# Kernel optimization log

Measured on AMD Instinct MI355X. Metric: run time of the kernel, lower is better.

## Reference

```python
import math
import jax, jax.numpy as jnp
import numpy as np

D_MODEL = 1024
N_HEADS = 16
D_HEAD = D_MODEL // N_HEADS


def get_alibi_slopes(n_heads: int) -> np.ndarray:
    def pow2_slopes(n):
        start = 2 ** (-2 ** (-(math.log2(n) - 3)))
        return np.array([start * start ** i for i in range(n)], dtype=np.float32)
    if math.log2(n_heads).is_integer():
        return pow2_slopes(n_heads)
    closest = 2 ** math.floor(math.log2(n_heads))
    slopes = pow2_slopes(closest)
    extra = pow2_slopes(2 * closest)[0::2][: n_heads - closest]
    return np.concatenate([slopes, extra], axis=0)


def setup_inputs() -> dict:
    key = jax.random.key(0)
    ks = jax.random.split(key, 9)
    B, S, D = 2, 2048, D_MODEL
    scale = 1.0 / math.sqrt(D)
    inp = {
        "x": jax.random.normal(ks[0], (B, S, D), dtype=jnp.float32),
        "Wq": jax.random.normal(ks[1], (D, D), dtype=jnp.float32) * scale,
        "bq": jnp.zeros((D,), dtype=jnp.float32),
        "Wk": jax.random.normal(ks[2], (D, D), dtype=jnp.float32) * scale,
        "bk": jnp.zeros((D,), dtype=jnp.float32),
        "Wv": jax.random.normal(ks[3], (D, D), dtype=jnp.float32) * scale,
        "bv": jnp.zeros((D,), dtype=jnp.float32),
        "Wo": jax.random.normal(ks[4], (D, D), dtype=jnp.float32) * scale,
        "bo": jnp.zeros((D,), dtype=jnp.float32),
    }
    return inp


def reference(x, Wq, bq, Wk, bk, Wv, bv, Wo, bo):
    B, S, D = x.shape
    H, Dh = N_HEADS, D_HEAD
    # projections (torch Linear: x @ W.T + b)
    q = (x @ Wq.T + bq).reshape(B, S, H, Dh).transpose(0, 2, 1, 3)  # [B,H,S,Dh]
    k = (x @ Wk.T + bk).reshape(B, S, H, Dh).transpose(0, 2, 1, 3)
    v = (x @ Wv.T + bv).reshape(B, S, H, Dh).transpose(0, 2, 1, 3)

    scores = jnp.einsum("bhqd,bhkd->bhqk", q, k) / math.sqrt(Dh)  # [B,H,S,S]

    slopes = jnp.asarray(get_alibi_slopes(H), dtype=scores.dtype)  # [H]
    pos = jnp.arange(S, dtype=scores.dtype)
    pos_diff = pos[None, :] - pos[:, None]                         # [S,S] (k - q)
    alibi = slopes[:, None, None] * pos_diff[None, :, :]           # [H,S,S]
    scores = scores + alibi[None]

    causal = jnp.tril(jnp.ones((S, S), dtype=bool))
    scores = jnp.where(causal[None, None], scores, -jnp.inf)

    weights = jax.nn.softmax(scores, axis=-1)
    y = jnp.einsum("bhqk,bhkd->bhqd", weights, v)                  # [B,H,S,Dh]
    y = y.transpose(0, 2, 1, 3).reshape(B, S, D)
    return y @ Wo.T + bo
```

## Files before the change

### kernel.cpp

```cpp
#include <hip/hip_runtime.h>

typedef unsigned short u16;
typedef unsigned int u32;
typedef short bf16x8 __attribute__((ext_vector_type(8)));
typedef float f32x4 __attribute__((ext_vector_type(4)));
typedef u16 u16x4 __attribute__((ext_vector_type(4)));

#define D_MODEL 1024
#define NHEADS 16
#define DHEAD 64
#define BATCH 2
#define SEQ 2048
#define NROWS (BATCH * SEQ)
#define NTILES (SEQ / 64)

static __device__ __forceinline__ u16 f2bf(float f) {
  u32 x = __float_as_uint(f);
  x += 0x7fffu + ((x >> 16) & 1u);
  return (u16)(x >> 16);
}

#define GLL16(gp, lp)                                             \
  __builtin_amdgcn_global_load_lds(                               \
      (const __attribute__((address_space(1))) u32*)(gp),         \
      (__attribute__((address_space(3))) u32*)(lp), 16, 0, 0)

__global__ __launch_bounds__(256) void castk(const float* __restrict__ in,
                                             u16* __restrict__ out, int n4) {
  int i = blockIdx.x * 256 + threadIdx.x;
  if (i >= n4) return;
  float4 v = ((const float4*)in)[i];
  u32 lo = (u32)f2bf(v.x) | ((u32)f2bf(v.y) << 16);
  u32 hi = (u32)f2bf(v.z) | ((u32)f2bf(v.w) << 16);
  ((uint2*)out)[i] = make_uint2(lo, hi);
}

__global__ __launch_bounds__(256) void castw(const float* __restrict__ w0,
                                             const float* __restrict__ w1,
                                             const float* __restrict__ w2,
                                             const float* __restrict__ w3,
                                             u16* __restrict__ o0,
                                             u16* __restrict__ o1,
                                             u16* __restrict__ o2,
                                             u16* __restrict__ o3) {
  const int z = blockIdx.z;
  const float* in = (z == 0) ? w0 : (z == 1) ? w1 : (z == 2) ? w2 : w3;
  u16* out = (z == 0) ? o0 : (z == 1) ? o1 : (z == 2) ? o2 : o3;
  int i = blockIdx.x * 256 + threadIdx.x;
  float4 v = ((const float4*)in)[i];
  u32 lo = (u32)f2bf(v.x) | ((u32)f2bf(v.y) << 16);
  u32 hi = (u32)f2bf(v.z) | ((u32)f2bf(v.w) << 16);
  ((uint2*)out)[i] = make_uint2(lo, hi);
}

template <int MODE>
__device__ __forceinline__ void gemm_core(const u16* __restrict__ A,
                                          const u16* __restrict__ Bw,
                                          const float* __restrict__ bias,
                                          u16* __restrict__ ob,
                                          float* __restrict__ of,
                                          int bm, int bn) {
  constexpr int K = 1024, N = 1024;
  __shared__ __attribute__((aligned(16))) u16 As[2][128 * 32];
  __shared__ __attribute__((aligned(16))) u16 Bs[2][128 * 32];
  const int tx = threadIdx.x;
  const int w = tx >> 6, lane = tx & 63;
  const int wm = w >> 1, wn = w & 1;
  const int c = lane & 15, g = lane >> 4;
  f32x4 acc[4][4];
  for (int m = 0; m < 4; ++m)
    for (int n = 0; n < 4; ++n) acc[m][n] = {0.f, 0.f, 0.f, 0.f};
  const int srow = w * 16 + (lane >> 2);
  const int sck = (lane & 3) * 8;
  for (int m = 0; m < 2; ++m) {
    GLL16(A + (size_t)(bm + m * 64 + srow) * K + sck,
          (char*)As[0] + m * 4096 + w * 1024);
    GLL16(Bw + (size_t)(bn + m * 64 + srow) * K + sck,
          (char*)Bs[0] + m * 4096 + w * 1024);
  }
  int cur = 0;
  for (int k0 = 0; k0 < K; k0 += 32) {
    __syncthreads();
    if (k0 + 32 < K) {
      for (int m = 0; m < 2; ++m) {
        GLL16(A + (size_t)(bm + m * 64 + srow) * K + k0 + 32 + sck,
              (char*)As[cur ^ 1] + m * 4096 + w * 1024);
        GLL16(Bw + (size_t)(bn + m * 64 + srow) * K + k0 + 32 + sck,
              (char*)Bs[cur ^ 1] + m * 4096 + w * 1024);
      }
    }
    bf16x8 af[4], bf_[4];
    for (int m = 0; m < 4; ++m)
      af[m] = *(const bf16x8*)(As[cur] + (wm * 64 + m * 16 + c) * 32 + g * 8);
    for (int n = 0; n < 4; ++n)
      bf_[n] = *(const bf16x8*)(Bs[cur] + (wn * 64 + n * 16 + c) * 32 + g * 8);
    for (int m = 0; m < 4; ++m)
      for (int n = 0; n < 4; ++n)
        acc[m][n] = __builtin_amdgcn_mfma_f32_16x16x32_bf16(af[m], bf_[n],
                                                            acc[m][n], 0, 0, 0);
    cur ^= 1;
  }
  for (int n = 0; n < 4; ++n) {
    const int col = bn + wn * 64 + n * 16 + c;
    const float bv = bias[col];
    for (int m = 0; m < 4; ++m) {
      if (MODE == 2) {
        const int rs = bm + wm * 64 + m * 16 + g * 4;
        u16x4 pk;
        for (int r = 0; r < 4; ++r) pk[r] = f2bf(acc[m][n][r] + bv);
        const size_t vrow = (size_t)((rs >> 11) * NHEADS + (col >> 6)) * DHEAD +
                            (col & 63);
        *(u16x4*)(ob + vrow * SEQ + (rs & 2047)) = pk;
      } else {
        for (int r = 0; r < 4; ++r) {
          const int row = bm + wm * 64 + m * 16 + g * 4 + r;
          float v = acc[m][n][r] + bv;
          if (MODE == 1)
            of[(size_t)row * N + col] = v;
          else
            ob[(size_t)row * N + col] = f2bf(v);
        }
      }
    }
  }
}

__global__ __launch_bounds__(256) void gemm_qkv(const u16* __restrict__ xb,
                                                const u16* __restrict__ wq,
                                                const u16* __restrict__ wk,
                                                const float* __restrict__ bq,
                                                const float* __restrict__ bk,
                                                u16* __restrict__ q,
                                                u16* __restrict__ k) {
  const int z = blockIdx.z;
  const u16* W = (z == 0) ? wq : wk;
  const float* bi = (z == 0) ? bq : bk;
  u16* o = (z == 0) ? q : k;
  gemm_core<0>(xb, W, bi, o, nullptr, blockIdx.y * 128, blockIdx.x * 128);
}

__global__ __launch_bounds__(256) void gemm_v(const u16* __restrict__ xb,
                                              const u16* __restrict__ wv,
                                              const float* __restrict__ bv,
                                              u16* __restrict__ vt) {
  gemm_core<2>(xb, wv, bv, vt, nullptr, blockIdx.y * 128, blockIdx.x * 128);
}

__global__ __launch_bounds__(256) void gemm_o(const u16* __restrict__ yb,
                                              const u16* __restrict__ wo,
                                              const float* __restrict__ bo,
                                              float* __restrict__ out) {
  gemm_core<1>(yb, wo, bo, nullptr, out, blockIdx.y * 128, blockIdx.x * 128);
}

__global__ __launch_bounds__(256) void attn(const u16* __restrict__ qb,
                                            const u16* __restrict__ kb,
                                            const u16* __restrict__ vt,
                                            u16* __restrict__ yb) {
  __shared__ __attribute__((aligned(16))) u16 Qs[64 * 64];
  __shared__ __attribute__((aligned(16))) u16 Ks[2][64 * 64];
  __shared__ __attribute__((aligned(16))) u16 Vs[2][64 * 64];
  __shared__ __attribute__((aligned(16))) u16 Ps[4 * 16 * 64];
  const int tx = threadIdx.x;
  const int w = tx >> 6, lane = tx & 63;
  const int c = lane & 15, g = lane >> 4;
  const int f = blockIdx.x;
  const int bh = (f & 7) * 4 + ((f >> 3) & 3);
  const int qi = NTILES - 1 - (f >> 5);
  const int b = bh >> 4, h = bh & 15;
  const int q0 = qi * 64;
  const size_t rb = (size_t)b * SEQ;
  const size_t vtb = (size_t)bh * DHEAD;
  const float slope2 = exp2f(-0.5f * (float)(h + 1)) * 1.44269504f;
  const float S2 = 0.125f * 1.44269504f;

  const int strow = w * 8 + (lane >> 3);
  const int stck = lane & 7;

  for (int m = 0; m < 2; ++m) {
    int row = m * 32 + strow;
    GLL16(qb + (rb + q0 + row) * D_MODEL + h * DHEAD + ((stck ^ (row & 7)) * 8),
          (char*)Qs + m * 4096 + w * 1024);
    GLL16(kb + (rb + row) * D_MODEL + h * DHEAD + ((stck ^ (row & 7)) * 8),
          (char*)Ks[0] + m * 4096 + w * 1024);
    GLL16(vt + (vtb + row) * SEQ + ((stck ^ (row & 7)) * 8),
          (char*)Vs[0] + m * 4096 + w * 1024);
  }

  float mrun[4];
  f32x4 acc[4], lacc;
  for (int r = 0; r < 4; ++r) mrun[r] = -1e30f;
  for (int d = 0; d < 4; ++d) acc[d] = {0.f, 0.f, 0.f, 0.f};
  lacc = {0.f, 0.f, 0.f, 0.f};
  bf16x8 ones;
  for (int j = 0; j < 8; ++j) ones[j] = (short)0x3F80;
  const float qrow[4] = {(float)(q0 + w * 16 + g * 4 + 0),
                         (float)(q0 + w * 16 + g * 4 + 1),
                         (float)(q0 + w * 16 + g * 4 + 2),
                         (float)(q0 + w * 16 + g * 4 + 3)};
  const int qrowi = q0 + w * 16 + g * 4;

  int cur = 0;
  for (int kt = 0; kt <= qi; ++kt) {
    __syncthreads();
    if (kt < qi) {
      for (int m = 0; m < 2; ++m) {
        int row = m * 32 + strow;
        GLL16(kb + (rb + (kt + 1) * 64 + row) * D_MODEL + h * DHEAD +
                  ((stck ^ (row & 7)) * 8),
              (char*)Ks[cur ^ 1] + m * 4096 + w * 1024);
        GLL16(vt + (vtb + row) * SEQ + (kt + 1) * 64 +
                  ((stck ^ (row & 7)) * 8),
              (char*)Vs[cur ^ 1] + m * 4096 + w * 1024);
      }
    }

    bf16x8 aq[2];
    for (int ks = 0; ks < 2; ++ks)
      aq[ks] = *(const bf16x8*)((const char*)Qs + (w * 16 + c) * 128 +
                                ((ks * 64 + g * 16) ^ ((c & 7) << 4)));
    f32x4 sc[4];
    for (int n = 0; n < 4; ++n) {
      sc[n] = {0.f, 0.f, 0.f, 0.f};
      for (int ks = 0; ks < 2; ++ks) {
        bf16x8 bk = *(const bf16x8*)((const char*)Ks[cur] + (n * 16 + c) * 128 +
                                     ((ks * 64 + g * 16) ^ ((c & 7) << 4)));
        sc[n] = __builtin_amdgcn_mfma_f32_16x16x32_bf16(aq[ks], bk, sc[n], 0, 0, 0);
      }
    }

    const int kbase = kt * 64 + c;
    const bool diag = (kt == qi);
    float p[4][4];
    for (int r = 0; r < 4; ++r) {
      const float base = slope2 * ((float)kbase - qrow[r]);
      float srow_[4];
      float rmax = -1e30f;
      for (int n = 0; n < 4; ++n) {
        float s = fmaf(sc[n][r], S2, base + slope2 * (float)(n * 16));
        if (diag && (kbase + n * 16 > qrowi + r)) s = -1e30f;
        srow_[n] = s;
        rmax = fmaxf(rmax, s);
      }
      for (int off = 1; off < 16; off <<= 1)
        rmax = fmaxf(rmax, __shfl_xor(rmax, off));
      const float mn = fmaxf(mrun[r], rmax);
      const float corr = exp2f(mrun[r] - mn);
      mrun[r] = mn;
      for (int n = 0; n < 4; ++n) p[n][r] = exp2f(srow_[n] - mn);
      lacc[r] *= corr;
      for (int d = 0; d < 4; ++d) acc[d][r] *= corr;
    }

    for (int n = 0; n < 4; ++n)
      for (int r = 0; r < 4; ++r) {
        const int row = g * 4 + r;
        *(u16*)((char*)Ps + w * 2048 + row * 128 +
                (((n * 16 + c) * 2) ^ ((row & 7) << 4))) = f2bf(p[n][r]);
      }

    for (int ks = 0; ks < 2; ++ks) {
      bf16x8 pa = *(const bf16x8*)((const char*)Ps + w * 2048 + c * 128 +
                                   ((ks * 64 + g * 16) ^ ((c & 7) << 4)));
      for (int d = 0; d < 4; ++d) {
        bf16x8 vb_ = *(const bf16x8*)((const char*)Vs[cur] +
                                      (d * 16 + c) * 128 +
                                      ((ks * 64 + g * 16) ^ ((c & 7) << 4)));
        acc[d] = __builtin_amdgcn_mfma_f32_16x16x32_bf16(pa, vb_, acc[d], 0, 0, 0);
      }
      lacc = __builtin_amdgcn_mfma_f32_16x16x32_bf16(pa, ones, lacc, 0, 0, 0);
    }
    cur ^= 1;
  }

  for (int d = 0; d < 4; ++d)
    for (int r = 0; r < 4; ++r) {
      const int qlocal = w * 16 + g * 4 + r;
      float o = acc[d][r] / lacc[r];
      yb[(rb + q0 + qlocal) * D_MODEL + h * DHEAD + d * 16 + c] = f2bf(o);
    }
}

extern "C" void kernel_launch(void* const* d_in, const int* in_sizes, int n_in,
                              void* d_out, int out_size, void* d_ws,
                              size_t ws_size, hipStream_t stream) {
  const float* x = (const float*)d_in[0];
  const float* Wq = (const float*)d_in[1];
  const float* bq = (const float*)d_in[2];
  const float* Wk = (const float*)d_in[3];
  const float* bk = (const float*)d_in[4];
  const float* Wv = (const float*)d_in[5];
  const float* bv = (const float*)d_in[6];
  const float* Wo = (const float*)d_in[7];
  const float* bo = (const float*)d_in[8];
  float* out = (float*)d_out;

  char* ws = (char*)d_ws;
  u16* xb = (u16*)(ws + (size_t)0);
  u16* wqb = (u16*)(ws + ((size_t)8 << 20));
  u16* wkb = (u16*)(ws + ((size_t)10 << 20));
  u16* wvb = (u16*)(ws + ((size_t)12 << 20));
  u16* wob = (u16*)(ws + ((size_t)14 << 20));
  u16* qb = (u16*)(ws + ((size_t)16 << 20));
  u16* kb = (u16*)(ws + ((size_t)24 << 20));
  u16* vtb = (u16*)(ws + ((size_t)32 << 20));
  u16* yb = xb;

  castk<<<4096, 256, 0, stream>>>(x, xb, NROWS * D_MODEL / 4);
  castw<<<dim3(1024, 1, 4), 256, 0, stream>>>(Wq, Wk, Wv, Wo, wqb, wkb, wvb,
                                              wob);

  gemm_qkv<<<dim3(8, 32, 2), 256, 0, stream>>>(xb, wqb, wkb, bq, bk, qb, kb);
  gemm_v<<<dim3(8, 32, 1), 256, 0, stream>>>(xb, wvb, bv, vtb);
  attn<<<dim3(NTILES * NHEADS * BATCH, 1, 1), 256, 0, stream>>>(qb, kb, vtb, yb);
  gemm_o<<<dim3(8, 32, 1), 256, 0, stream>>>(yb, wob, bo, out);
}
```

Baseline: 228.1 us.

## Merge V projection into QKV launch and transpose score MFMA in attention

```diff
diff --git a/kernel.cpp b/kernel.cpp
--- a/kernel.cpp
+++ b/kernel.cpp
@@ -18,6 +18,12 @@
   u32 x = __float_as_uint(f);
   x += 0x7fffu + ((x >> 16) & 1u);
   return (u16)(x >> 16);
+}
+
+static __device__ __forceinline__ u32 cvtpk(float lo, float hi) {
+  u32 r;
+  asm("v_cvt_pk_bf16_f32 %0, %1, %2" : "=v"(r) : "v"(lo), "v"(hi));
+  return r;
 }
 
 #define GLL16(gp, lp)                                             \
@@ -128,22 +134,19 @@
 __global__ __launch_bounds__(256) void gemm_qkv(const u16* __restrict__ xb,
                                                 const u16* __restrict__ wq,
                                                 const u16* __restrict__ wk,
+                                                const u16* __restrict__ wv,
                                                 const float* __restrict__ bq,
                                                 const float* __restrict__ bk,
+                                                const float* __restrict__ bv,
                                                 u16* __restrict__ q,
-                                                u16* __restrict__ k) {
+                                                u16* __restrict__ k,
+                                                u16* __restrict__ vt) {
   const int z = blockIdx.z;
-  const u16* W = (z == 0) ? wq : wk;
-  const float* bi = (z == 0) ? bq : bk;
-  u16* o = (z == 0) ? q : k;
-  gemm_core<0>(xb, W, bi, o, nullptr, blockIdx.y * 128, blockIdx.x * 128);
-}
-
-__global__ __launch_bounds__(256) void gemm_v(const u16* __restrict__ xb,
-                                              const u16* __restrict__ wv,
-                                              const float* __restrict__ bv,
-                                              u16* __restrict__ vt) {
-  gemm_core<2>(xb, wv, bv, vt, nullptr, blockIdx.y * 128, blockIdx.x * 128);
+  if (z == 2)
+    gemm_core<2>(xb, wv, bv, vt, nullptr, blockIdx.y * 128, blockIdx.x * 128);
+  else
+    gemm_core<0>(xb, z ? wk : wq, z ? bk : bq, z ? k : q, nullptr,
+                 blockIdx.y * 128, blockIdx.x * 128);
 }
 
 __global__ __launch_bounds__(256) void gemm_o(const u16* __restrict__ yb,
@@ -157,7 +160,6 @@
                                             const u16* __restrict__ kb,
                                             const u16* __restrict__ vt,
                                             u16* __restrict__ yb) {
-  __shared__ __attribute__((aligned(16))) u16 Qs[64 * 64];
   __shared__ __attribute__((aligned(16))) u16 Ks[2][64 * 64];
   __shared__ __attribute__((aligned(16))) u16 Vs[2][64 * 64];
   __shared__ __attribute__((aligned(16))) u16 Ps[4 * 16 * 64];
@@ -177,28 +179,28 @@
   const int strow = w * 8 + (lane >> 3);
   const int stck = lane & 7;
 
+  const u16* qp = qb + (rb + q0 + w * 16 + c) * D_MODEL + h * DHEAD;
+  bf16x8 aq[2];
+  aq[0] = *(const bf16x8*)(qp + g * 8);
+  aq[1] = *(const bf16x8*)(qp + 32 + g * 8);
+
   for (int m = 0; m < 2; ++m) {
     int row = m * 32 + strow;
-    GLL16(qb + (rb + q0 + row) * D_MODEL + h * DHEAD + ((stck ^ (row & 7)) * 8),
-          (char*)Qs + m * 4096 + w * 1024);
     GLL16(kb + (rb + row) * D_MODEL + h * DHEAD + ((stck ^ (row & 7)) * 8),
           (char*)Ks[0] + m * 4096 + w * 1024);
     GLL16(vt + (vtb + row) * SEQ + ((stck ^ (row & 7)) * 8),
           (char*)Vs[0] + m * 4096 + w * 1024);
   }
 
-  float mrun[4];
+  float mrun = -1e30f;
   f32x4 acc[4], lacc;
-  for (int r = 0; r < 4; ++r) mrun[r] = -1e30f;
   for (int d = 0; d < 4; ++d) acc[d] = {0.f, 0.f, 0.f, 0.f};
   lacc = {0.f, 0.f, 0.f, 0.f};
   bf16x8 ones;
   for (int j = 0; j < 8; ++j) ones[j] = (short)0x3F80;
-  const float qrow[4] = {(float)(q0 + w * 16 + g * 4 + 0),
-                         (float)(q0 + w * 16 + g * 4 + 1),
-                         (float)(q0 + w * 16 + g * 4 + 2),
-                         (float)(q0 + w * 16 + g * 4 + 3)};
-  const int qrowi = q0 + w * 16 + g * 4;
+  const int qidx = q0 + w * 16 + c;
+  const float alibase = slope2 * (float)(4 * g - qidx);
+  const int swz = (c & 7) << 4;
 
   int cur = 0;
   for (int kt = 0; kt <= qi; ++kt) {
@@ -215,57 +217,55 @@
       }
     }
 
-    bf16x8 aq[2];
-    for (int ks = 0; ks < 2; ++ks)
-      aq[ks] = *(const bf16x8*)((const char*)Qs + (w * 16 + c) * 128 +
-                                ((ks * 64 + g * 16) ^ ((c & 7) << 4)));
     f32x4 sc[4];
     for (int n = 0; n < 4; ++n) {
       sc[n] = {0.f, 0.f, 0.f, 0.f};
       for (int ks = 0; ks < 2; ++ks) {
         bf16x8 bk = *(const bf16x8*)((const char*)Ks[cur] + (n * 16 + c) * 128 +
-                                     ((ks * 64 + g * 16) ^ ((c & 7) << 4)));
-        sc[n] = __builtin_amdgcn_mfma_f32_16x16x32_bf16(aq[ks], bk, sc[n], 0, 0, 0);
-      }
-    }
-
-    const int kbase = kt * 64 + c;
+                                     ((ks * 64 + g * 16) ^ swz));
+        sc[n] = __builtin_amdgcn_mfma_f32_16x16x32_bf16(bk, aq[ks], sc[n], 0, 0, 0);
+      }
+    }
+
     const bool diag = (kt == qi);
+    const int kb0 = kt * 64 + 4 * g;
+    const float alikt = alibase + slope2 * (float)(kt * 64);
     float p[4][4];
+    float rmax = -1e30f;
+    for (int n = 0; n < 4; ++n) {
+      const float tn = alikt + slope2 * (float)(n * 16);
+      for (int r = 0; r < 4; ++r) {
+        float s = fmaf(sc[n][r], S2, fmaf((float)r, slope2, tn));
+        if (diag && (kb0 + n * 16 + r > qidx)) s = -1e30f;
+        p[n][r] = s;
+        rmax = fmaxf(rmax, s);
+      }
+    }
+    rmax = fmaxf(rmax, __shfl_xor(rmax, 16));
+    rmax = fmaxf(rmax, __shfl_xor(rmax, 32));
+    const float mn = fmaxf(mrun, rmax);
+    const float corr = exp2f(mrun - mn);
+    mrun = mn;
+    for (int n = 0; n < 4; ++n) {
+      u32 lo = cvtpk(exp2f(p[n][0] - mn), exp2f(p[n][1] - mn));
+      u32 hi = cvtpk(exp2f(p[n][2] - mn), exp2f(p[n][3] - mn));
+      *(uint2*)((char*)Ps + w * 2048 + c * 128 + ((n * 32 + 8 * g) ^ swz)) =
+          make_uint2(lo, hi);
+    }
+    float corr_row[4];
+    for (int r = 0; r < 4; ++r) corr_row[r] = __shfl(corr, 4 * g + r);
     for (int r = 0; r < 4; ++r) {
-      const float base = slope2 * ((float)kbase - qrow[r]);
-      float srow_[4];
-      float rmax = -1e30f;
-      for (int n = 0; n < 4; ++n) {
-        float s = fmaf(sc[n][r], S2, base + slope2 * (float)(n * 16));
-        if (diag && (kbase + n * 16 > qrowi + r)) s = -1e30f;
-        srow_[n] = s;
-        rmax = fmaxf(rmax, s);
-      }
-      for (int off = 1; off < 16; off <<= 1)
-        rmax = fmaxf(rmax, __shfl_xor(rmax, off));
-      const float mn = fmaxf(mrun[r], rmax);
-      const float corr = exp2f(mrun[r] - mn);
-      mrun[r] = mn;
-      for (int n = 0; n < 4; ++n) p[n][r] = exp2f(srow_[n] - mn);
-      lacc[r] *= corr;
-      for (int d = 0; d < 4; ++d) acc[d][r] *= corr;
-    }
-
-    for (int n = 0; n < 4; ++n)
-      for (int r = 0; r < 4; ++r) {
-        const int row = g * 4 + r;
-        *(u16*)((char*)Ps + w * 2048 + row * 128 +
-                (((n * 16 + c) * 2) ^ ((row & 7) << 4))) = f2bf(p[n][r]);
-      }
+      lacc[r] *= corr_row[r];
+      for (int d = 0; d < 4; ++d) acc[d][r] *= corr_row[r];
+    }
 
     for (int ks = 0; ks < 2; ++ks) {
       bf16x8 pa = *(const bf16x8*)((const char*)Ps + w * 2048 + c * 128 +
-                                   ((ks * 64 + g * 16) ^ ((c & 7) << 4)));
+                                   ((ks * 64 + g * 16) ^ swz));
       for (int d = 0; d < 4; ++d) {
         bf16x8 vb_ = *(const bf16x8*)((const char*)Vs[cur] +
                                       (d * 16 + c) * 128 +
-                                      ((ks * 64 + g * 16) ^ ((c & 7) << 4)));
+                                      ((ks * 64 + g * 16) ^ swz));
         acc[d] = __builtin_amdgcn_mfma_f32_16x16x32_bf16(pa, vb_, acc[d], 0, 0, 0);
       }
       lacc = __builtin_amdgcn_mfma_f32_16x16x32_bf16(pa, ones, lacc, 0, 0, 0);
@@ -310,8 +310,8 @@
   castw<<<dim3(1024, 1, 4), 256, 0, stream>>>(Wq, Wk, Wv, Wo, wqb, wkb, wvb,
                                               wob);
 
-  gemm_qkv<<<dim3(8, 32, 2), 256, 0, stream>>>(xb, wqb, wkb, bq, bk, qb, kb);
-  gemm_v<<<dim3(8, 32, 1), 256, 0, stream>>>(xb, wvb, bv, vtb);
+  gemm_qkv<<<dim3(8, 32, 3), 256, 0, stream>>>(xb, wqb, wkb, wvb, bq, bk, bv,
+                                               qb, kb, vtb);
   attn<<<dim3(NTILES * NHEADS * BATCH, 1, 1), 256, 0, stream>>>(qb, kb, vtb, yb);
   gemm_o<<<dim3(8, 32, 1), 256, 0, stream>>>(yb, wob, bo, out);
 }
```

Result: faster. 210.8 us (-7.6%).
